# Optimization experiments

Measured on AMD Instinct MI355X. Metric: run time of the kernel, lower is better.

The kernel has to match this reference:

```python
import jax, jax.numpy as jnp
import numpy as np

EMBED_DIM = 256
UNITS = 512


def setup_inputs() -> dict:
    key = jax.random.key(0)
    ks = jax.random.split(key, 8)
    B, L = 2048, 64  # batch, 8*8 spatial locations
    features = jax.random.normal(ks[0], (B, L, EMBED_DIM), dtype=jnp.float32)
    hidden = jax.random.normal(ks[1], (B, UNITS), dtype=jnp.float32)
    s1 = 1.0 / np.sqrt(EMBED_DIM)
    s2 = 1.0 / np.sqrt(UNITS)
    W1 = jax.random.normal(ks[2], (EMBED_DIM, UNITS), dtype=jnp.float32) * s1
    b1 = jnp.zeros((UNITS,), dtype=jnp.float32)
    W2 = jax.random.normal(ks[3], (UNITS, UNITS), dtype=jnp.float32) * s2
    b2 = jnp.zeros((UNITS,), dtype=jnp.float32)
    V = jax.random.normal(ks[4], (UNITS, 1), dtype=jnp.float32) * s2
    bv = jnp.zeros((1,), dtype=jnp.float32)
    return {"features": features, "hidden": hidden, "W1": W1, "b1": b1,
            "W2": W2, "b2": b2, "V": V, "bv": bv}


def reference(features, hidden, W1, b1, W2, b2, V, bv):
    # features: [B, L, E], hidden: [B, U]
    # Bahdanau additive attention
    proj_f = jnp.einsum('ble,eu->blu', features, W1) + b1          # [B, L, U]
    proj_h = (hidden @ W2 + b2)[:, None, :]                        # [B, 1, U]
    e = jnp.tanh(proj_f + proj_h)                                  # [B, L, U]
    score = jnp.einsum('blu,uo->blo', e, V) + bv                   # [B, L, 1]
    attention_weights = jax.nn.softmax(score, axis=1)              # [B, L, 1]
    context_vector = jnp.sum(attention_weights * features, axis=1) # [B, E]
    return context_vector, attention_weights
```

## Files before the change

kernel.cpp:

```cpp
#include <hip/hip_runtime.h>
#include <math.h>

#define BATCH 2048
#define LDIM 64
#define EDIM 256
#define UDIM 512

typedef __attribute__((ext_vector_type(8))) _Float16 half8;
typedef __attribute__((ext_vector_type(4))) float floatx4;

__device__ inline float tanh_fast(float x) {
    float t = __builtin_amdgcn_exp2f(x * 2.88539008177792681f);
    return 1.f - 2.f * __builtin_amdgcn_rcpf(t + 1.f);
}
__device__ inline half8 cvt8(float4 f0, float4 f1) {
    half8 h;
    h[0] = (_Float16)f0.x; h[1] = (_Float16)f0.y;
    h[2] = (_Float16)f0.z; h[3] = (_Float16)f0.w;
    h[4] = (_Float16)f1.x; h[5] = (_Float16)f1.y;
    h[6] = (_Float16)f1.z; h[7] = (_Float16)f1.w;
    return h;
}
__device__ inline const half8* bfrag(const unsigned short* F, int kc, int ntg, int l) {
    return (const half8*)(F + ((((size_t)kc * 32 + ntg) * 64 + l) << 3));
}

__global__ __launch_bounds__(256) void prep_frag(const float* __restrict__ W1,
                                                 const float* __restrict__ W2,
                                                 unsigned short* __restrict__ F1,
                                                 unsigned short* __restrict__ F2) {
    __shared__ float S[32 * 128];
    int bid = blockIdx.x;
    const float* W; unsigned short* F; int kc, grp;
    if (bid < 32) { W = W1; F = F1; kc = bid >> 2; grp = bid & 3; }
    else { bid -= 32; W = W2; F = F2; kc = bid >> 2; grp = bid & 3; }
    const int tid = threadIdx.x;
    const float* src = W + (size_t)kc * 32 * UDIM + grp * 128;
    float4* Sv = (float4*)S;
#pragma unroll
    for (int i = 0; i < 4; ++i) {
        int f = tid + i * 256;
        int k = f >> 5, c4 = f & 31;
        Sv[f] = *(const float4*)(src + (size_t)k * UDIM + c4 * 4);
    }
    __syncthreads();
#pragma unroll
    for (int i = 0; i < 2; ++i) {
        int u = tid + i * 256;
        int lane = u & 63, ntl = u >> 6;
        int n_loc = ntl * 16 + (lane & 15);
        int k0 = (lane >> 4) * 8;
        half8 h;
#pragma unroll
        for (int j = 0; j < 8; ++j)
            h[j] = (_Float16)S[(k0 + j) * 128 + n_loc];
        int ntg = grp * 8 + ntl;
        *(half8*)(F + (((size_t)kc * 32 + ntg) * 64 + lane) * 8) = h;
    }
}

__global__ __launch_bounds__(256) void prep_ph(const float* __restrict__ hidden,
                                               const unsigned short* __restrict__ F2,
                                               const float* __restrict__ b1,
                                               const float* __restrict__ b2,
                                               float* __restrict__ ph) {
    const int tid = threadIdx.x;
    const int w = tid >> 6;
    const int l = tid & 63;
    const int r0 = blockIdx.x * 16;

    floatx4 acc[8];
#pragma unroll
    for (int i = 0; i < 8; ++i) acc[i] = (floatx4){0.f, 0.f, 0.f, 0.f};

    const float* ap = hidden + (size_t)(r0 + (l & 15)) * UDIM + ((l >> 4) << 3);

    float4 a0 = *(const float4*)(ap);
    float4 a1 = *(const float4*)(ap + 4);
    half8 B[8];
#pragma unroll
    for (int nt = 0; nt < 8; ++nt) B[nt] = *bfrag(F2, 0, w * 8 + nt, l);

    for (int kc = 0; kc < 16; ++kc) {
        half8 a = cvt8(a0, a1);
        float4 n0, n1; half8 NB[8];
        if (kc < 15) {
            n0 = *(const float4*)(ap + (kc + 1) * 32);
            n1 = *(const float4*)(ap + (kc + 1) * 32 + 4);
#pragma unroll
            for (int nt = 0; nt < 8; ++nt) NB[nt] = *bfrag(F2, kc + 1, w * 8 + nt, l);
        }
#pragma unroll
        for (int nt = 0; nt < 8; ++nt)
            acc[nt] = __builtin_amdgcn_mfma_f32_16x16x32_f16(a, B[nt], acc[nt], 0, 0, 0);
        if (kc < 15) {
            a0 = n0; a1 = n1;
#pragma unroll
            for (int nt = 0; nt < 8; ++nt) B[nt] = NB[nt];
        }
    }
#pragma unroll
    for (int nt = 0; nt < 8; ++nt) {
        const int n = (w * 8 + nt) * 16 + (l & 15);
        const float bias = b1[n] + b2[n];
#pragma unroll
        for (int r = 0; r < 4; ++r) {
            const int m = (l >> 4) * 4 + r;
            ph[(size_t)(r0 + m) * UDIM + n] = acc[nt][r] + bias;
        }
    }
}

__global__ __launch_bounds__(512, 4) void attn_main(
    const float* __restrict__ feat, const unsigned short* __restrict__ F1,
    const float* __restrict__ ph, const float* __restrict__ Vw,
    const float* __restrict__ bv,
    float* __restrict__ ctx_out, float* __restrict__ w_out)
{
    __shared__ unsigned short lA[8 * 4 * 64 * 8];
    __shared__ float phl[512];
    __shared__ float Vl[512];
    __shared__ float scp[8][64];
    __shared__ float wsm[64];
    __shared__ float ctxp[2][256];

    const int tid = threadIdx.x;
    const int w = tid >> 6;
    const int l = tid & 63;
    const size_t b = blockIdx.x;
    const float* fb = feat + b * (LDIM * EDIM);

    float4 f4[2][4];
#pragma unroll
    for (int p = 0; p < 2; ++p) {
        const int u = tid + 512 * p;
        const float4* gp = (const float4*)(fb + (u >> 4) * EDIM + (u & 15) * 16);
        f4[p][0] = gp[0]; f4[p][1] = gp[1]; f4[p][2] = gp[2]; f4[p][3] = gp[3];
    }
    phl[tid] = ph[b * UDIM + tid];
    Vl[tid]  = Vw[tid];

#pragma unroll
    for (int p = 0; p < 2; ++p) {
        const int u  = tid + 512 * p;
        const int r  = u >> 4, kc = (u & 15) >> 1, o = (u & 1) * 2;
        const int mt = r >> 4, rr = r & 15;
        const int base = (kc * 4 + mt) * 64;
        *(half8*)&lA[(base + ((o * 16 + rr) ^ kc)) * 8]       = cvt8(f4[p][0], f4[p][1]);
        *(half8*)&lA[(base + (((o + 1) * 16 + rr) ^ kc)) * 8] = cvt8(f4[p][2], f4[p][3]);
    }

    floatx4 acc[4][4];
#pragma unroll
    for (int i = 0; i < 4; ++i)
#pragma unroll
        for (int j = 0; j < 4; ++j) acc[i][j] = (floatx4){0.f, 0.f, 0.f, 0.f};

    __syncthreads();

    for (int kc = 0; kc < 8; ++kc) {
        half8 Bc[4];
#pragma unroll
        for (int nt = 0; nt < 4; ++nt) Bc[nt] = *bfrag(F1, kc, w * 4 + nt, l);
        half8 a[4];
#pragma unroll
        for (int mt = 0; mt < 4; ++mt)
            a[mt] = *(const half8*)&lA[((kc * 4 + mt) * 64 + (l ^ kc)) * 8];
#pragma unroll
        for (int nt = 0; nt < 4; ++nt)
#pragma unroll
            for (int mt = 0; mt < 4; ++mt)
                acc[nt][mt] = __builtin_amdgcn_mfma_f32_16x16x32_f16(
                    a[mt], Bc[nt], acc[nt][mt], 0, 0, 0);
    }

    float sv[4][4];
#pragma unroll
    for (int mt = 0; mt < 4; ++mt)
#pragma unroll
        for (int r = 0; r < 4; ++r) sv[mt][r] = 0.f;
#pragma unroll
    for (int nt = 0; nt < 4; ++nt) {
        const int n = (w * 4 + nt) * 16 + (l & 15);
        const float phn = phl[n];
        const float vn  = Vl[n];
#pragma unroll
        for (int mt = 0; mt < 4; ++mt)
#pragma unroll
            for (int r = 0; r < 4; ++r)
                sv[mt][r] += tanh_fast(acc[nt][mt][r] + phn) * vn;
    }
#pragma unroll
    for (int mt = 0; mt < 4; ++mt)
#pragma unroll
        for (int r = 0; r < 4; ++r) {
            float v = sv[mt][r];
            v += __shfl_xor(v, 1);
            v += __shfl_xor(v, 2);
            v += __shfl_xor(v, 4);
            v += __shfl_xor(v, 8);
            if ((l & 15) == 0) scp[w][mt * 16 + (l >> 4) * 4 + r] = v;
        }
    __syncthreads();

    if (tid < 64) {
        float s = bv[0];
#pragma unroll
        for (int wv = 0; wv < 8; ++wv) s += scp[wv][tid];
        float m = s;
        m = fmaxf(m, __shfl_xor(m, 32));
        m = fmaxf(m, __shfl_xor(m, 16));
        m = fmaxf(m, __shfl_xor(m, 8));
        m = fmaxf(m, __shfl_xor(m, 4));
        m = fmaxf(m, __shfl_xor(m, 2));
        m = fmaxf(m, __shfl_xor(m, 1));
        float e = __builtin_amdgcn_exp2f((s - m) * 1.44269504088896341f);
        float sum = e;
        sum += __shfl_xor(sum, 32);
        sum += __shfl_xor(sum, 16);
        sum += __shfl_xor(sum, 8);
        sum += __shfl_xor(sum, 4);
        sum += __shfl_xor(sum, 2);
        sum += __shfl_xor(sum, 1);
        float wgt = e / sum;
        wsm[tid] = wgt;
        w_out[b * LDIM + tid] = wgt;
    }
    __syncthreads();

    {
        const int e = tid & 255, h = tid >> 8;
        float c = 0.f;
#pragma unroll 8
        for (int ll = h * 32; ll < h * 32 + 32; ++ll)
            c = fmaf(wsm[ll], fb[ll * EDIM + e], c);
        ctxp[h][e] = c;
    }
    __syncthreads();
    if (tid < 256)
        ctx_out[b * EDIM + tid] = ctxp[0][tid] + ctxp[1][tid];
}

extern "C" void kernel_launch(void* const* d_in, const int* in_sizes, int n_in,
                              void* d_out, int out_size, void* d_ws, size_t ws_size,
                              hipStream_t stream) {
    const float* features = (const float*)d_in[0];
    const float* hidden   = (const float*)d_in[1];
    const float* W1       = (const float*)d_in[2];
    const float* b1       = (const float*)d_in[3];
    const float* W2       = (const float*)d_in[4];
    const float* b2       = (const float*)d_in[5];
    const float* Vw       = (const float*)d_in[6];
    const float* bv       = (const float*)d_in[7];

    float* ctx_out = (float*)d_out;
    float* w_out   = (float*)d_out + (size_t)BATCH * EDIM;

    float* ph = (float*)d_ws;
    unsigned short* F1 = (unsigned short*)(ph + (size_t)BATCH * UDIM);
    unsigned short* F2 = F1 + (size_t)8 * 32 * 64 * 8;

    prep_frag<<<dim3(96), dim3(256), 0, stream>>>(W1, W2, F1, F2);
    prep_ph<<<dim3(128), dim3(256), 0, stream>>>(hidden, F2, b1, b2, ph);
    attn_main<<<dim3(BATCH), dim3(512), 0, stream>>>(
        features, F1, ph, Vw, bv, ctx_out, w_out);
}
```

Measured before the change: 261.0 us.

## Process four batches per block with register-prefetched feature tiles

The main kernel now handles four batch elements per block in a loop instead of one. The next batch's features are loaded into registers during the current batch's score and softmax phases, then written to LDS after the context pass. V and the hidden projection are read straight into registers rather than staged through shared memory. This hides global load latency and spreads block setup over more work, but it cuts the grid to 512 blocks, which may leave parts of the 256-CU device underused, and it adds register pressure.

```diff
diff --git a/kernel.cpp b/kernel.cpp
--- a/kernel.cpp
+++ b/kernel.cpp
@@ -111,6 +111,26 @@
     }
 }
 
+__device__ inline void ld_feat(const float* __restrict__ fb, int tid, float4 f4[2][4]) {
+#pragma unroll
+    for (int p = 0; p < 2; ++p) {
+        const int u = tid + 512 * p;
+        const float4* gp = (const float4*)(fb + (u >> 4) * EDIM + (u & 15) * 16);
+        f4[p][0] = gp[0]; f4[p][1] = gp[1]; f4[p][2] = gp[2]; f4[p][3] = gp[3];
+    }
+}
+__device__ inline void st_lA(unsigned short* lA, int tid, const float4 f4[2][4]) {
+#pragma unroll
+    for (int p = 0; p < 2; ++p) {
+        const int u  = tid + 512 * p;
+        const int r  = u >> 4, kc = (u & 15) >> 1, o = (u & 1) * 2;
+        const int mt = r >> 4, rr = r & 15;
+        const int base = (kc * 4 + mt) * 64;
+        *(half8*)&lA[(base + ((o * 16 + rr) ^ kc)) * 8]       = cvt8(f4[p][0], f4[p][1]);
+        *(half8*)&lA[(base + (((o + 1) * 16 + rr) ^ kc)) * 8] = cvt8(f4[p][2], f4[p][3]);
+    }
+}
+
 __global__ __launch_bounds__(512, 4) void attn_main(
     const float* __restrict__ feat, const unsigned short* __restrict__ F1,
     const float* __restrict__ ph, const float* __restrict__ Vw,
@@ -118,8 +138,6 @@
     float* __restrict__ ctx_out, float* __restrict__ w_out)
 {
     __shared__ unsigned short lA[8 * 4 * 64 * 8];
-    __shared__ float phl[512];
-    __shared__ float Vl[512];
     __shared__ float scp[8][64];
     __shared__ float wsm[64];
     __shared__ float ctxp[2][256];
@@ -127,118 +145,124 @@
     const int tid = threadIdx.x;
     const int w = tid >> 6;
     const int l = tid & 63;
-    const size_t b = blockIdx.x;
-    const float* fb = feat + b * (LDIM * EDIM);
+    const size_t b0 = (size_t)blockIdx.x * 4;
+
+    const float bvv = bv[0];
+    float vnr[4];
+#pragma unroll
+    for (int nt = 0; nt < 4; ++nt)
+        vnr[nt] = Vw[(w * 4 + nt) * 16 + (l & 15)];
 
     float4 f4[2][4];
-#pragma unroll
-    for (int p = 0; p < 2; ++p) {
-        const int u = tid + 512 * p;
-        const float4* gp = (const float4*)(fb + (u >> 4) * EDIM + (u & 15) * 16);
-        f4[p][0] = gp[0]; f4[p][1] = gp[1]; f4[p][2] = gp[2]; f4[p][3] = gp[3];
-    }
-    phl[tid] = ph[b * UDIM + tid];
-    Vl[tid]  = Vw[tid];
-
-#pragma unroll
-    for (int p = 0; p < 2; ++p) {
-        const int u  = tid + 512 * p;
-        const int r  = u >> 4, kc = (u & 15) >> 1, o = (u & 1) * 2;
-        const int mt = r >> 4, rr = r & 15;
-        const int base = (kc * 4 + mt) * 64;
-        *(half8*)&lA[(base + ((o * 16 + rr) ^ kc)) * 8]       = cvt8(f4[p][0], f4[p][1]);
-        *(half8*)&lA[(base + (((o + 1) * 16 + rr) ^ kc)) * 8] = cvt8(f4[p][2], f4[p][3]);
-    }
-
-    floatx4 acc[4][4];
-#pragma unroll
-    for (int i = 0; i < 4; ++i)
-#pragma unroll
-        for (int j = 0; j < 4; ++j) acc[i][j] = (floatx4){0.f, 0.f, 0.f, 0.f};
-
+    ld_feat(feat + b0 * (LDIM * EDIM), tid, f4);
+    st_lA(lA, tid, f4);
     __syncthreads();
 
-    for (int kc = 0; kc < 8; ++kc) {
-        half8 Bc[4];
-#pragma unroll
-        for (int nt = 0; nt < 4; ++nt) Bc[nt] = *bfrag(F1, kc, w * 4 + nt, l);
-        half8 a[4];
+    for (int i = 0; i < 4; ++i) {
+        const size_t b = b0 + i;
+        const float* fbi = feat + b * (LDIM * EDIM);
+
+        float phv[4];
+#pragma unroll
+        for (int nt = 0; nt < 4; ++nt)
+            phv[nt] = ph[b * UDIM + (w * 4 + nt) * 16 + (l & 15)];
+
+        floatx4 acc[4][4];
+#pragma unroll
+        for (int x = 0; x < 4; ++x)
+#pragma unroll
+            for (int y = 0; y < 4; ++y) acc[x][y] = (floatx4){0.f, 0.f, 0.f, 0.f};
+
+        for (int kc = 0; kc < 8; ++kc) {
+            half8 Bc[4];
+#pragma unroll
+            for (int nt = 0; nt < 4; ++nt) Bc[nt] = *bfrag(F1, kc, w * 4 + nt, l);
+            half8 a[4];
+#pragma unroll
+            for (int mt = 0; mt < 4; ++mt)
+                a[mt] = *(const half8*)&lA[((kc * 4 + mt) * 64 + (l ^ kc)) * 8];
+#pragma unroll
+            for (int nt = 0; nt < 4; ++nt)
+#pragma unroll
+                for (int mt = 0; mt < 4; ++mt)
+                    acc[nt][mt] = __builtin_amdgcn_mfma_f32_16x16x32_f16(
+                        a[mt], Bc[nt], acc[nt][mt], 0, 0, 0);
+        }
+
+        float sv[4][4];
 #pragma unroll
         for (int mt = 0; mt < 4; ++mt)
-            a[mt] = *(const half8*)&lA[((kc * 4 + mt) * 64 + (l ^ kc)) * 8];
-#pragma unroll
-        for (int nt = 0; nt < 4; ++nt)
+#pragma unroll
+            for (int r = 0; r < 4; ++r) sv[mt][r] = 0.f;
+#pragma unroll
+        for (int nt = 0; nt < 4; ++nt) {
+            const float phn = phv[nt];
+            const float vn  = vnr[nt];
 #pragma unroll
             for (int mt = 0; mt < 4; ++mt)
-                acc[nt][mt] = __builtin_amdgcn_mfma_f32_16x16x32_f16(
-                    a[mt], Bc[nt], acc[nt][mt], 0, 0, 0);
-    }
-
-    float sv[4][4];
-#pragma unroll
-    for (int mt = 0; mt < 4; ++mt)
-#pragma unroll
-        for (int r = 0; r < 4; ++r) sv[mt][r] = 0.f;
-#pragma unroll
-    for (int nt = 0; nt < 4; ++nt) {
-        const int n = (w * 4 + nt) * 16 + (l & 15);
-        const float phn = phl[n];
-        const float vn  = Vl[n];
+#pragma unroll
+                for (int r = 0; r < 4; ++r)
+                    sv[mt][r] += tanh_fast(acc[nt][mt][r] + phn) * vn;
+        }
 #pragma unroll
         for (int mt = 0; mt < 4; ++mt)
 #pragma unroll
-            for (int r = 0; r < 4; ++r)
-                sv[mt][r] += tanh_fast(acc[nt][mt][r] + phn) * vn;
-    }
-#pragma unroll
-    for (int mt = 0; mt < 4; ++mt)
-#pragma unroll
-        for (int r = 0; r < 4; ++r) {
-            float v = sv[mt][r];
-            v += __shfl_xor(v, 1);
-            v += __shfl_xor(v, 2);
-            v += __shfl_xor(v, 4);
-            v += __shfl_xor(v, 8);
-            if ((l & 15) == 0) scp[w][mt * 16 + (l >> 4) * 4 + r] = v;
-        }
-    __syncthreads();
-
-    if (tid < 64) {
-        float s = bv[0];
-#pragma unroll
-        for (int wv = 0; wv < 8; ++wv) s += scp[wv][tid];
-        float m = s;
-        m = fmaxf(m, __shfl_xor(m, 32));
-        m = fmaxf(m, __shfl_xor(m, 16));
-        m = fmaxf(m, __shfl_xor(m, 8));
-        m = fmaxf(m, __shfl_xor(m, 4));
-        m = fmaxf(m, __shfl_xor(m, 2));
-        m = fmaxf(m, __shfl_xor(m, 1));
-        float e = __builtin_amdgcn_exp2f((s - m) * 1.44269504088896341f);
-        float sum = e;
-        sum += __shfl_xor(sum, 32);
-        sum += __shfl_xor(sum, 16);
-        sum += __shfl_xor(sum, 8);
-        sum += __shfl_xor(sum, 4);
-        sum += __shfl_xor(sum, 2);
-        sum += __shfl_xor(sum, 1);
-        float wgt = e / sum;
-        wsm[tid] = wgt;
-        w_out[b * LDIM + tid] = wgt;
-    }
-    __syncthreads();
-
-    {
-        const int e = tid & 255, h = tid >> 8;
-        float c = 0.f;
+            for (int r = 0; r < 4; ++r) {
+                float v = sv[mt][r];
+                v += __shfl_xor(v, 1);
+                v += __shfl_xor(v, 2);
+                v += __shfl_xor(v, 4);
+                v += __shfl_xor(v, 8);
+                if ((l & 15) == 0) scp[w][mt * 16 + (l >> 4) * 4 + r] = v;
+            }
+
+        if (i < 3)
+            ld_feat(feat + (b + 1) * (LDIM * EDIM), tid, f4);
+
+        __syncthreads();
+
+        if (tid < 64) {
+            float s = bvv;
+#pragma unroll
+            for (int wv = 0; wv < 8; ++wv) s += scp[wv][tid];
+            float m = s;
+            m = fmaxf(m, __shfl_xor(m, 32));
+            m = fmaxf(m, __shfl_xor(m, 16));
+            m = fmaxf(m, __shfl_xor(m, 8));
+            m = fmaxf(m, __shfl_xor(m, 4));
+            m = fmaxf(m, __shfl_xor(m, 2));
+            m = fmaxf(m, __shfl_xor(m, 1));
+            float e = __builtin_amdgcn_exp2f((s - m) * 1.44269504088896341f);
+            float sum = e;
+            sum += __shfl_xor(sum, 32);
+            sum += __shfl_xor(sum, 16);
+            sum += __shfl_xor(sum, 8);
+            sum += __shfl_xor(sum, 4);
+            sum += __shfl_xor(sum, 2);
+            sum += __shfl_xor(sum, 1);
+            float wgt = e / sum;
+            wsm[tid] = wgt;
+            w_out[b * LDIM + tid] = wgt;
+        }
+        __syncthreads();
+
+        {
+            const int e = tid & 255, h = tid >> 8;
+            float c = 0.f;
 #pragma unroll 8
-        for (int ll = h * 32; ll < h * 32 + 32; ++ll)
-            c = fmaf(wsm[ll], fb[ll * EDIM + e], c);
-        ctxp[h][e] = c;
-    }
-    __syncthreads();
-    if (tid < 256)
-        ctx_out[b * EDIM + tid] = ctxp[0][tid] + ctxp[1][tid];
+            for (int ll = h * 32; ll < h * 32 + 32; ++ll)
+                c = fmaf(wsm[ll], fbi[ll * EDIM + e], c);
+            ctxp[h][e] = c;
+        }
+
+        if (i < 3)
+            st_lA(lA, tid, f4);
+
+        __syncthreads();
+
+        if (tid < 256)
+            ctx_out[b * EDIM + tid] = ctxp[0][tid] + ctxp[1][tid];
+    }
 }
 
 extern "C" void kernel_launch(void* const* d_in, const int* in_sizes, int n_in,
@@ -262,6 +286,6 @@
 
     prep_frag<<<dim3(96), dim3(256), 0, stream>>>(W1, W2, F1, F2);
     prep_ph<<<dim3(128), dim3(256), 0, stream>>>(hidden, F2, b1, b2, ph);
-    attn_main<<<dim3(BATCH), dim3(512), 0, stream>>>(
+    attn_main<<<dim3(512), dim3(512), 0, stream>>>(
         features, F1, ph, Vw, bv, ctx_out, w_out);
 }
```

After: 470.3 us. 1.8x slower.

## Split MFMA accumulation into two N-chunks, raise occupancy, drop softmax barriers

Applied to the files above, without the earlier changes.

The main attention kernel now computes its projection tile in two halves of N, holding only 8 accumulators instead of 16, and applies tanh/V reduction per half. This lowers register pressure so the launch bound can ask for 6 blocks per CU instead of 4. Every wave now redundantly computes the softmax and broadcasts weights with shuffles, and the context reduction uses a cross-half shuffle. Two __syncthreads and the wsm/ctxp shared arrays go away. The costs are redundant softmax work in all waves and MFMA chains that are less deep, and the higher occupancy target may cause spills.

```diff
diff --git a/kernel.cpp b/kernel.cpp
--- a/kernel.cpp
+++ b/kernel.cpp
@@ -111,7 +111,7 @@
     }
 }
 
-__global__ __launch_bounds__(512, 4) void attn_main(
+__global__ __launch_bounds__(512, 6) void attn_main(
     const float* __restrict__ feat, const unsigned short* __restrict__ F1,
     const float* __restrict__ ph, const float* __restrict__ Vw,
     const float* __restrict__ bv,
@@ -121,14 +121,14 @@
     __shared__ float phl[512];
     __shared__ float Vl[512];
     __shared__ float scp[8][64];
-    __shared__ float wsm[64];
-    __shared__ float ctxp[2][256];
 
     const int tid = threadIdx.x;
     const int w = tid >> 6;
     const int l = tid & 63;
     const size_t b = blockIdx.x;
     const float* fb = feat + b * (LDIM * EDIM);
+
+    const float bvv = bv[0];
 
     float4 f4[2][4];
 #pragma unroll
@@ -150,46 +150,48 @@
         *(half8*)&lA[(base + (((o + 1) * 16 + rr) ^ kc)) * 8] = cvt8(f4[p][2], f4[p][3]);
     }
 
-    floatx4 acc[4][4];
-#pragma unroll
-    for (int i = 0; i < 4; ++i)
-#pragma unroll
-        for (int j = 0; j < 4; ++j) acc[i][j] = (floatx4){0.f, 0.f, 0.f, 0.f};
-
     __syncthreads();
 
-    for (int kc = 0; kc < 8; ++kc) {
-        half8 Bc[4];
-#pragma unroll
-        for (int nt = 0; nt < 4; ++nt) Bc[nt] = *bfrag(F1, kc, w * 4 + nt, l);
-        half8 a[4];
-#pragma unroll
-        for (int mt = 0; mt < 4; ++mt)
-            a[mt] = *(const half8*)&lA[((kc * 4 + mt) * 64 + (l ^ kc)) * 8];
-#pragma unroll
-        for (int nt = 0; nt < 4; ++nt)
+    float sv[4][4];
+#pragma unroll
+    for (int mt = 0; mt < 4; ++mt)
+#pragma unroll
+        for (int r = 0; r < 4; ++r) sv[mt][r] = 0.f;
+
+    for (int nc = 0; nc < 2; ++nc) {
+        floatx4 acc[2][4];
+#pragma unroll
+        for (int x = 0; x < 2; ++x)
+#pragma unroll
+            for (int y = 0; y < 4; ++y) acc[x][y] = (floatx4){0.f, 0.f, 0.f, 0.f};
+
+        for (int kc = 0; kc < 8; ++kc) {
+            half8 Bc[2];
+#pragma unroll
+            for (int nt = 0; nt < 2; ++nt)
+                Bc[nt] = *bfrag(F1, kc, w * 4 + nc * 2 + nt, l);
+#pragma unroll
+            for (int mt = 0; mt < 4; ++mt) {
+                const half8 a = *(const half8*)&lA[((kc * 4 + mt) * 64 + (l ^ kc)) * 8];
+#pragma unroll
+                for (int nt = 0; nt < 2; ++nt)
+                    acc[nt][mt] = __builtin_amdgcn_mfma_f32_16x16x32_f16(
+                        a, Bc[nt], acc[nt][mt], 0, 0, 0);
+            }
+        }
+#pragma unroll
+        for (int nt = 0; nt < 2; ++nt) {
+            const int n = (w * 4 + nc * 2 + nt) * 16 + (l & 15);
+            const float phn = phl[n];
+            const float vn  = Vl[n];
 #pragma unroll
             for (int mt = 0; mt < 4; ++mt)
-                acc[nt][mt] = __builtin_amdgcn_mfma_f32_16x16x32_f16(
-                    a[mt], Bc[nt], acc[nt][mt], 0, 0, 0);
-    }
-
-    float sv[4][4];
-#pragma unroll
-    for (int mt = 0; mt < 4; ++mt)
-#pragma unroll
-        for (int r = 0; r < 4; ++r) sv[mt][r] = 0.f;
-#pragma unroll
-    for (int nt = 0; nt < 4; ++nt) {
-        const int n = (w * 4 + nt) * 16 + (l & 15);
-        const float phn = phl[n];
-        const float vn  = Vl[n];
-#pragma unroll
-        for (int mt = 0; mt < 4; ++mt)
-#pragma unroll
-            for (int r = 0; r < 4; ++r)
-                sv[mt][r] += tanh_fast(acc[nt][mt][r] + phn) * vn;
-    }
+#pragma unroll
+                for (int r = 0; r < 4; ++r)
+                    sv[mt][r] += tanh_fast(acc[nt][mt][r] + phn) * vn;
+        }
+    }
+
 #pragma unroll
     for (int mt = 0; mt < 4; ++mt)
 #pragma unroll
@@ -203,42 +205,41 @@
         }
     __syncthreads();
 
-    if (tid < 64) {
-        float s = bv[0];
-#pragma unroll
-        for (int wv = 0; wv < 8; ++wv) s += scp[wv][tid];
-        float m = s;
-        m = fmaxf(m, __shfl_xor(m, 32));
-        m = fmaxf(m, __shfl_xor(m, 16));
-        m = fmaxf(m, __shfl_xor(m, 8));
-        m = fmaxf(m, __shfl_xor(m, 4));
-        m = fmaxf(m, __shfl_xor(m, 2));
-        m = fmaxf(m, __shfl_xor(m, 1));
-        float e = __builtin_amdgcn_exp2f((s - m) * 1.44269504088896341f);
-        float sum = e;
-        sum += __shfl_xor(sum, 32);
-        sum += __shfl_xor(sum, 16);
-        sum += __shfl_xor(sum, 8);
-        sum += __shfl_xor(sum, 4);
-        sum += __shfl_xor(sum, 2);
-        sum += __shfl_xor(sum, 1);
-        float wgt = e / sum;
-        wsm[tid] = wgt;
-        w_out[b * LDIM + tid] = wgt;
-    }
-    __syncthreads();
+    float s = bvv;
+#pragma unroll
+    for (int wv = 0; wv < 8; ++wv) s += scp[wv][l];
+    float m = s;
+    m = fmaxf(m, __shfl_xor(m, 32));
+    m = fmaxf(m, __shfl_xor(m, 16));
+    m = fmaxf(m, __shfl_xor(m, 8));
+    m = fmaxf(m, __shfl_xor(m, 4));
+    m = fmaxf(m, __shfl_xor(m, 2));
+    m = fmaxf(m, __shfl_xor(m, 1));
+    float e = __builtin_amdgcn_exp2f((s - m) * 1.44269504088896341f);
+    float sum = e;
+    sum += __shfl_xor(sum, 32);
+    sum += __shfl_xor(sum, 16);
+    sum += __shfl_xor(sum, 8);
+    sum += __shfl_xor(sum, 4);
+    sum += __shfl_xor(sum, 2);
+    sum += __shfl_xor(sum, 1);
+    const float wgt = e / sum;
+    if (w == 0) w_out[b * LDIM + l] = wgt;
 
     {
-        const int e = tid & 255, h = tid >> 8;
+        const int e0 = (w << 5) + (l & 31);
+        const int h  = l >> 5;
         float c = 0.f;
 #pragma unroll 8
-        for (int ll = h * 32; ll < h * 32 + 32; ++ll)
-            c = fmaf(wsm[ll], fb[ll * EDIM + e], c);
-        ctxp[h][e] = c;
-    }
-    __syncthreads();
-    if (tid < 256)
-        ctx_out[b * EDIM + tid] = ctxp[0][tid] + ctxp[1][tid];
+        for (int r = 0; r < 32; ++r) {
+            const int ll = h * 32 + r;
+            const float wl = __shfl(wgt, ll);
+            c = fmaf(wl, fb[ll * EDIM + e0], c);
+        }
+        c += __shfl_xor(c, 32);
+        if (l < 32)
+            ctx_out[b * EDIM + e0] = c;
+    }
 }
 
 extern "C" void kernel_launch(void* const* d_in, const int* in_sizes, int n_in,
```

Measured after the change: 491.8 us. +88.4%, slower.

## Double-buffer feature tile in LDS per K-chunk to overlap loads with MFMA

Applied to the files above, without the earlier changes.

Replaces the up-front load of the whole 64x256 feature tile into a 32KB LDS buffer with a two-slot ring of one K-chunk each. The next chunk's global load is issued before the current chunk's MFMAs and written to LDS afterwards, overlapping memory latency with compute. LDS use drops sharply, which could allow more resident blocks, but it adds seven extra block-wide barriers per block.

```diff
diff --git a/kernel.cpp b/kernel.cpp
--- a/kernel.cpp
+++ b/kernel.cpp
@@ -7,6 +7,7 @@
 #define UDIM 512
 
 typedef __attribute__((ext_vector_type(8))) _Float16 half8;
+typedef __attribute__((ext_vector_type(4))) _Float16 half4;
 typedef __attribute__((ext_vector_type(4))) float floatx4;
 
 __device__ inline float tanh_fast(float x) {
@@ -19,6 +20,12 @@
     h[2] = (_Float16)f0.z; h[3] = (_Float16)f0.w;
     h[4] = (_Float16)f1.x; h[5] = (_Float16)f1.y;
     h[6] = (_Float16)f1.z; h[7] = (_Float16)f1.w;
+    return h;
+}
+__device__ inline half4 cvt4(float4 f) {
+    half4 h;
+    h[0] = (_Float16)f.x; h[1] = (_Float16)f.y;
+    h[2] = (_Float16)f.z; h[3] = (_Float16)f.w;
     return h;
 }
 __device__ inline const half8* bfrag(const unsigned short* F, int kc, int ntg, int l) {
@@ -117,7 +124,7 @@
     const float* __restrict__ bv,
     float* __restrict__ ctx_out, float* __restrict__ w_out)
 {
-    __shared__ unsigned short lA[8 * 4 * 64 * 8];
+    __shared__ _Float16 lS[2][4][64][8];
     __shared__ float phl[512];
     __shared__ float Vl[512];
     __shared__ float scp[8][64];
@@ -130,25 +137,18 @@
     const size_t b = blockIdx.x;
     const float* fb = feat + b * (LDIM * EDIM);
 
-    float4 f4[2][4];
-#pragma unroll
-    for (int p = 0; p < 2; ++p) {
-        const int u = tid + 512 * p;
-        const float4* gp = (const float4*)(fb + (u >> 4) * EDIM + (u & 15) * 16);
-        f4[p][0] = gp[0]; f4[p][1] = gp[1]; f4[p][2] = gp[2]; f4[p][3] = gp[3];
-    }
-    phl[tid] = ph[b * UDIM + tid];
-    Vl[tid]  = Vw[tid];
-
-#pragma unroll
-    for (int p = 0; p < 2; ++p) {
-        const int u  = tid + 512 * p;
-        const int r  = u >> 4, kc = (u & 15) >> 1, o = (u & 1) * 2;
-        const int mt = r >> 4, rr = r & 15;
-        const int base = (kc * 4 + mt) * 64;
-        *(half8*)&lA[(base + ((o * 16 + rr) ^ kc)) * 8]       = cvt8(f4[p][0], f4[p][1]);
-        *(half8*)&lA[(base + (((o + 1) * 16 + rr) ^ kc)) * 8] = cvt8(f4[p][2], f4[p][3]);
-    }
+    const int r  = tid >> 3, q = tid & 7;
+    const int mt_s = r >> 4;
+    const int fl   = (q >> 1) * 16 + (r & 15);
+    const int h4   = (q & 1) * 4;
+
+    {
+        float4 g = *(const float4*)(fb + r * EDIM + q * 4);
+        phl[tid] = ph[b * UDIM + tid];
+        Vl[tid]  = Vw[tid];
+        *(half4*)&lS[0][mt_s][fl ^ 0][h4] = cvt4(g);
+    }
+    __syncthreads();
 
     floatx4 acc[4][4];
 #pragma unroll
@@ -156,29 +156,34 @@
 #pragma unroll
         for (int j = 0; j < 4; ++j) acc[i][j] = (floatx4){0.f, 0.f, 0.f, 0.f};
 
-    __syncthreads();
-
     for (int kc = 0; kc < 8; ++kc) {
+        float4 g;
+        if (kc < 7)
+            g = *(const float4*)(fb + r * EDIM + (kc + 1) * 32 + q * 4);
+
         half8 Bc[4];
 #pragma unroll
         for (int nt = 0; nt < 4; ++nt) Bc[nt] = *bfrag(F1, kc, w * 4 + nt, l);
-        half8 a[4];
-#pragma unroll
-        for (int mt = 0; mt < 4; ++mt)
-            a[mt] = *(const half8*)&lA[((kc * 4 + mt) * 64 + (l ^ kc)) * 8];
-#pragma unroll
-        for (int nt = 0; nt < 4; ++nt)
-#pragma unroll
-            for (int mt = 0; mt < 4; ++mt)
+#pragma unroll
+        for (int mt = 0; mt < 4; ++mt) {
+            const half8 a = *(const half8*)&lS[kc & 1][mt][l ^ kc][0];
+#pragma unroll
+            for (int nt = 0; nt < 4; ++nt)
                 acc[nt][mt] = __builtin_amdgcn_mfma_f32_16x16x32_f16(
-                    a[mt], Bc[nt], acc[nt][mt], 0, 0, 0);
+                    a, Bc[nt], acc[nt][mt], 0, 0, 0);
+        }
+
+        if (kc < 7) {
+            *(half4*)&lS[(kc + 1) & 1][mt_s][fl ^ (kc + 1)][h4] = cvt4(g);
+            __syncthreads();
+        }
     }
 
     float sv[4][4];
 #pragma unroll
     for (int mt = 0; mt < 4; ++mt)
 #pragma unroll
-        for (int r = 0; r < 4; ++r) sv[mt][r] = 0.f;
+        for (int rr = 0; rr < 4; ++rr) sv[mt][rr] = 0.f;
 #pragma unroll
     for (int nt = 0; nt < 4; ++nt) {
         const int n = (w * 4 + nt) * 16 + (l & 15);
@@ -187,19 +192,19 @@
 #pragma unroll
         for (int mt = 0; mt < 4; ++mt)
 #pragma unroll
-            for (int r = 0; r < 4; ++r)
-                sv[mt][r] += tanh_fast(acc[nt][mt][r] + phn) * vn;
+            for (int rr = 0; rr < 4; ++rr)
+                sv[mt][rr] += tanh_fast(acc[nt][mt][rr] + phn) * vn;
     }
 #pragma unroll
     for (int mt = 0; mt < 4; ++mt)
 #pragma unroll
-        for (int r = 0; r < 4; ++r) {
-            float v = sv[mt][r];
+        for (int rr = 0; rr < 4; ++rr) {
+            float v = sv[mt][rr];
             v += __shfl_xor(v, 1);
             v += __shfl_xor(v, 2);
             v += __shfl_xor(v, 4);
             v += __shfl_xor(v, 8);
-            if ((l & 15) == 0) scp[w][mt * 16 + (l >> 4) * 4 + r] = v;
+            if ((l & 15) == 0) scp[w][mt * 16 + (l >> 4) * 4 + rr] = v;
         }
     __syncthreads();
 
```

New measurement: 255.3 us. -2.2%, faster.
